# Kernel optimization log

Hardware: AMD Instinct MI355X
Metric: run time of the kernel (lower is better)

The kernel has to match this reference:

```python
import jax, jax.numpy as jnp
import numpy as np

EMBED_DIM = 1024
NUM_HEADS = 16
HEAD_DIM = EMBED_DIM // NUM_HEADS
NEG = -1000000000.0


def setup_inputs() -> dict:
    key = jax.random.key(0)
    ks = jax.random.split(key, 13)
    B, S, D = 4, 2048, EMBED_DIM
    scale = 1.0 / np.sqrt(D)
    inp = {
        "query": jax.random.normal(ks[0], (B, S, D), jnp.float32),
        "key": jax.random.normal(ks[1], (B, S, D), jnp.float32),
        "value": jax.random.normal(ks[2], (B, S, D), jnp.float32),
        "mask": jax.random.randint(ks[3], (B, 1, 1, S), 0, 2, jnp.int32),
        "Wq": jax.random.normal(ks[4], (D, D), jnp.float32) * scale,
        "bq": jnp.zeros((D,), jnp.float32),
        "Wk": jax.random.normal(ks[5], (D, D), jnp.float32) * scale,
        "bk": jnp.zeros((D,), jnp.float32),
        "Wv": jax.random.normal(ks[6], (D, D), jnp.float32) * scale,
        "bv": jnp.zeros((D,), jnp.float32),
        "Wo": jax.random.normal(ks[7], (D, D), jnp.float32) * scale,
        "bo": jnp.zeros((D,), jnp.float32),
    }
    return inp


def _split_heads(x):
    B, S, D = x.shape
    return x.reshape(B, S, NUM_HEADS, HEAD_DIM).transpose(0, 2, 1, 3)  # [B,H,S,hd]


def reference(query, key, value, mask, Wq, bq, Wk, bk, Wv, bv, Wo, bo):
    B, S, D = query.shape
    Q = _split_heads(query @ Wq + bq)
    K = _split_heads(key @ Wk + bk)
    V = _split_heads(value @ Wv + bv)
    scores = jnp.einsum("bhqd,bhkd->bhqk", Q, K) / jnp.sqrt(jnp.float32(HEAD_DIM))
    scores = jnp.where(mask == 0, jnp.float32(NEG), scores)
    attn = jax.nn.softmax(scores, axis=-1)
    out = jnp.einsum("bhqk,bhkd->bhqd", attn, V)
    out = out.transpose(0, 2, 1, 3).reshape(B, S, D)
    return out @ Wo + bo
```

## Files before the change

### kernel.cpp

```cpp
#include <hip/hip_runtime.h>


#define SEQ   2048
#define EDIM  1024
#define NHEAD 16
#define HDIM  64
#define NBAT  4
#define MTOK  8192

typedef __attribute__((ext_vector_type(8))) __bf16 bf16x8;
typedef __attribute__((ext_vector_type(4))) __bf16 bf16x4;
typedef __attribute__((ext_vector_type(4))) float f32x4;
typedef __attribute__((ext_vector_type(16))) float f32x16;
typedef __attribute__((ext_vector_type(8))) unsigned short us8;
typedef unsigned short u16;

#define SCL   0.1803368801111244f

__device__ __forceinline__ u16 bfbits(float f) {
    __bf16 h = (__bf16)f;
    return __builtin_bit_cast(u16, h);
}
__device__ __forceinline__ bf16x8 bc(us8 v) { return __builtin_bit_cast(bf16x8, v); }
__device__ __forceinline__ float exp2fast(float x) {
    float r;
    asm("v_exp_f32 %0, %1" : "=v"(r) : "v"(x));
    return r;
}
__device__ __forceinline__ void glds16(const void* g, void* l) {
    __builtin_amdgcn_global_load_lds(
        (const __attribute__((address_space(1))) unsigned int*)g,
        (__attribute__((address_space(3))) unsigned int*)l, 16, 0, 0);
}
#define VMCNT(n) asm volatile("s_waitcnt vmcnt(" #n ")" ::: "memory")

__global__ __launch_bounds__(256) void prep_kernel(const int* __restrict__ mask,
                                                   int* __restrict__ idxl,
                                                   int* __restrict__ cntp) {
    __shared__ int psum[257];
    const int b = blockIdx.x, t = threadIdx.x;
    const int* mp = mask + b * SEQ;
    int m8[8]; int s = 0;
#pragma unroll
    for (int i = 0; i < 8; ++i) { m8[i] = mp[t * 8 + i]; s += (m8[i] != 0); }
    psum[t + 1] = s;
    __syncthreads();
    if (t == 0) { psum[0] = 0; for (int i = 1; i <= 256; ++i) psum[i] += psum[i - 1]; }
    __syncthreads();
    int ex = psum[t];
#pragma unroll
    for (int i = 0; i < 8; ++i)
        if (m8[i] != 0) idxl[b * SEQ + (ex++)] = t * 8 + i;
    if (t == 0) cntp[b] = psum[256];
}

__global__ __launch_bounds__(256) void wtrans4_kernel(const float* __restrict__ W0,
                                                      const float* __restrict__ W1,
                                                      const float* __restrict__ W2,
                                                      const float* __restrict__ W3,
                                                      u16* __restrict__ WT) {
    __shared__ float tile[32][33];
    const int tx = threadIdx.x, ty = threadIdx.y;
    const int bx = blockIdx.x,  by = blockIdx.y, wz = blockIdx.z;
    const float* W = (wz == 0) ? W0 : (wz == 1) ? W1 : (wz == 2) ? W2 : W3;
    u16* O = WT + (size_t)wz * EDIM * EDIM;
#pragma unroll
    for (int i = 0; i < 4; ++i)
        tile[ty + i * 8][tx] = W[(size_t)(by * 32 + ty + i * 8) * EDIM + bx * 32 + tx];
    __syncthreads();
#pragma unroll
    for (int i = 0; i < 4; ++i) {
        int n = bx * 32 + ty + i * 8;
        int k = by * 32 + tx;
        O[(size_t)n * EDIM + k] = bfbits(tile[tx][ty + i * 8]);
    }
}

template <int MODE, bool AFP32, bool GATHER>
__global__ __launch_bounds__(256) void gemm_kernel(const void* __restrict__ Ap,
                                                   const u16* __restrict__ WT,
                                                   const float* __restrict__ bias,
                                                   void* __restrict__ outp,
                                                   const int* __restrict__ idxl,
                                                   const int* __restrict__ cntp,
                                                   const float oscale) {
    const int bm = blockIdx.x, bn = blockIdx.y;
    int cn = 0;
    if constexpr (GATHER) {
        cn = cntp[bm >> 4];
        if (((bm & 15) * 128) >= cn) return;
    }

    constexpr int ASZ = 128 * 32 * (AFP32 ? 4 : 2);
    __shared__ __align__(16) char Asraw[3][ASZ];
    __shared__ __align__(16) u16 Bs[3][128][32];

    const int tid  = threadIdx.x;
    const int lane = tid & 63, w = tid >> 6;
    const int g    = lane >> 4, l15 = lane & 15;
    const int wrow = w >> 1, wcol = w & 1;

    const char* pa[4];
    if constexpr (AFP32) {
        const float* A = (const float*)Ap;
#pragma unroll
        for (int t = 0; t < 4; ++t) {
            const int rloc = w * 32 + t * 8 + (lane >> 3);
            int arow;
            if constexpr (GATHER) {
                const int sloc = (bm & 15) * 128 + rloc;
                const int gi = (sloc < cn) ? idxl[(bm >> 4) * SEQ + sloc] : 0;
                arow = (bm >> 4) * SEQ + gi;
            } else arow = bm * 128 + rloc;
            const int scol = ((lane & 7) ^ (lane >> 3)) * 4;
            pa[t] = (const char*)(A + (size_t)arow * EDIM + scol);
        }
    } else {
        const u16* A = (const u16*)Ap;
#pragma unroll
        for (int t = 0; t < 2; ++t) {
            const int rloc = w * 32 + t * 16 + (lane >> 2);
            const int arow = bm * 128 + rloc;
            const int scol = ((lane & 3) ^ ((lane >> 3) & 3)) * 8;
            pa[t] = (const char*)(A + (size_t)arow * EDIM + scol);
        }
    }
    const char* pb[2];
#pragma unroll
    for (int t = 0; t < 2; ++t) {
        const int rloc = w * 32 + t * 16 + (lane >> 2);
        const int brow = bn * 128 + rloc;
        const int scol = ((lane & 3) ^ ((lane >> 3) & 3)) * 8;
        pb[t] = (const char*)(WT + (size_t)brow * EDIM + scol);
    }

    auto STAGE = [&](int bufn, int ko) {
        char* abase = &Asraw[bufn][0] + w * (AFP32 ? 4096 : 2048);
        if constexpr (AFP32) {
#pragma unroll
            for (int t = 0; t < 4; ++t)
                glds16(pa[t] + (size_t)ko * 4, abase + t * 1024);
        } else {
#pragma unroll
            for (int t = 0; t < 2; ++t)
                glds16(pa[t] + (size_t)ko * 2, abase + t * 1024);
        }
        char* bbase = (char*)&Bs[bufn][0][0] + w * 2048;
#pragma unroll
        for (int t = 0; t < 2; ++t)
            glds16(pb[t] + (size_t)ko * 2, bbase + t * 1024);
    };

    f32x4 acc[4][4] = {};
    constexpr int NT = EDIM / 32;

    STAGE(0, 0);
    STAGE(1, 32);
    if constexpr (AFP32) VMCNT(6); else VMCNT(4);
    __builtin_amdgcn_s_barrier();

    int bcur = 0, bn1 = 1, bn2 = 2;
#pragma unroll 1
    for (int kt = 0; kt < NT; ++kt) {
        if (kt + 2 < NT) STAGE(bn2, (kt + 2) * 32);

        bf16x8 af[4], bfr[4];
        if constexpr (AFP32) {
            const float* As = (const float*)&Asraw[bcur][0];
            const int x = l15 & 7;
#pragma unroll
            for (int i = 0; i < 4; ++i) {
                const int row = wrow * 64 + i * 16 + l15;
                f32x4 u0 = *(const f32x4*)(As + row * 32 + (((2 * g)     ^ x) * 4));
                f32x4 u1 = *(const f32x4*)(As + row * 32 + (((2 * g + 1) ^ x) * 4));
#pragma unroll
                for (int j = 0; j < 4; ++j) {
                    af[i][j]     = (__bf16)u0[j];
                    af[i][4 + j] = (__bf16)u1[j];
                }
            }
        } else {
            const u16* As = (const u16*)&Asraw[bcur][0];
            const int x = (l15 >> 1) & 3;
#pragma unroll
            for (int i = 0; i < 4; ++i) {
                const int row = wrow * 64 + i * 16 + l15;
                af[i] = bc(*(const us8*)(As + row * 32 + ((g ^ x) * 8)));
            }
        }
        {
            const int x = (l15 >> 1) & 3;
#pragma unroll
            for (int j = 0; j < 4; ++j) {
                const int row = wcol * 64 + j * 16 + l15;
                bfr[j] = bc(*(const us8*)((const u16*)&Bs[bcur][0][0] + row * 32 + ((g ^ x) * 8)));
            }
        }

#pragma unroll
        for (int i = 0; i < 4; ++i)
#pragma unroll
            for (int j = 0; j < 4; ++j)
                acc[i][j] = __builtin_amdgcn_mfma_f32_16x16x32_bf16(af[i], bfr[j], acc[i][j], 0, 0, 0);

        if (kt + 1 < NT) {
            if (kt + 2 < NT) {
                if constexpr (AFP32) VMCNT(6); else VMCNT(4);
            } else {
                VMCNT(0);
            }
            __builtin_amdgcn_s_barrier();
        }
        const int t = bcur; bcur = bn1; bn1 = bn2; bn2 = t;
    }

#pragma unroll
    for (int i = 0; i < 4; ++i) {
#pragma unroll
        for (int j = 0; j < 4; ++j) {
            const int gm0 = bm * 128 + wrow * 64 + i * 16 + g * 4;
            const int gn  = bn * 128 + wcol * 64 + j * 16 + l15;
            const float bv = bias[gn];
#pragma unroll
            for (int r = 0; r < 4; ++r) {
                float val = (acc[i][j][r] + bv) * oscale;
                const int m = gm0 + r;
                if constexpr (GATHER) {
                    if ((m & 2047) >= cn) val = 0.f;
                }
                if constexpr (MODE == 2) {
                    ((float*)outp)[(size_t)m * EDIM + gn] = val;
                } else {
                    const int b = m >> 11, s = m & 2047;
                    const int h = gn >> 6, d = gn & 63;
                    u16* O = (u16*)outp;
                    if constexpr (MODE == 0)
                        O[((size_t)(b * NHEAD + h) << 17) + s * HDIM + d] = bfbits(val);
                    else
                        O[((size_t)(b * NHEAD + h) << 17) + d * SEQ + s] = bfbits(val);
                }
            }
        }
    }
}

__global__ __launch_bounds__(256) void attn_kernel(const u16* __restrict__ Q,
                                                   const u16* __restrict__ K,
                                                   const u16* __restrict__ VT,
                                                   const int* __restrict__ cntp,
                                                   u16* __restrict__ O) {
    __shared__ u16 Klds[3][64][64];
    __shared__ u16 Vlds[3][64][64];

    const int tid = threadIdx.x, lane = tid & 63, w = tid >> 6;
    const int h = lane >> 5, l31 = lane & 31;

    const int id  = blockIdx.x;
    const int bh  = (id & 7) * 8 + ((id >> 3) >> 4);
    const int qb  = (id >> 3) & 15;
    const int b   = bh >> 4, hd_ = bh & 15;

    const u16* Qp = Q + ((size_t)bh << 17);
    const u16* Kp = K + ((size_t)bh << 17);
    const u16* Vp = VT + ((size_t)bh << 17);
    const int q0w = qb * 128 + w * 32;

    const int cn  = cntp[b];
    const int ktc = (cn + 63) >> 6;

    bf16x8 qf[4];
#pragma unroll
    for (int khd = 0; khd < 4; ++khd)
        qf[khd] = bc(*(const us8*)&Qp[(size_t)(q0w + l31) * HDIM + khd * 16 + h * 8]);

    const int b_  = l31 & 3, hp = (l31 >> 2) & 1, cc = l31 >> 3;
    const int piR = 16 * (cc & 1) + 8 * hp + 4 * (cc >> 1) + b_;
    const int swk = (piR & 3) ^ (((piR >> 3) & 3) << 1);
    const int swv = l31 & 7;

    const int lr = lane >> 3, lg = lane & 7;
    const u16* pKs[2]; const u16* pVs[2];
#pragma unroll
    for (int t = 0; t < 2; ++t) {
        const int rloc = w * 16 + t * 8 + lr;
        const int xk = (rloc & 3) ^ (((rloc >> 3) & 3) << 1);
        pKs[t] = Kp + (size_t)rloc * HDIM + ((lg ^ xk) << 3);
        const int xv = rloc & 7;
        pVs[t] = Vp + (size_t)rloc * SEQ + ((lg ^ xv) << 3);
    }

    auto STAGE = [&](int bufn, int kb) {
#pragma unroll
        for (int t = 0; t < 2; ++t) {
            glds16(pKs[t] + (size_t)kb * HDIM, &Klds[bufn][w * 16 + t * 8][0]);
            glds16(pVs[t] + kb,                &Vlds[bufn][w * 16 + t * 8][0]);
        }
    };

    f32x16 ot[2] = {};
    f32x16 ls = {};

    bf16x8 onesf;
#pragma unroll
    for (int j = 0; j < 8; ++j) onesf[j] = (__bf16)1.0f;

    STAGE(0, 0);
    if (ktc > 1) { STAGE(1, 64); VMCNT(4); } else { VMCNT(0); }
    __builtin_amdgcn_s_barrier();

    int bcur = 0, bn1 = 1, bn2 = 2;
    for (int kt = 0; kt < ktc; ++kt) {
        if (kt + 2 < ktc) STAGE(bn2, (kt + 2) * 64);

        f32x16 st[2] = {};
        __builtin_amdgcn_s_setprio(1);
#pragma unroll
        for (int kb2 = 0; kb2 < 2; ++kb2) {
            const u16* Kr = &Klds[bcur][kb2 * 32 + piR][0];
#pragma unroll
            for (int khd = 0; khd < 4; ++khd) {
                bf16x8 kf = bc(*(const us8*)&Kr[(khd * 16 + h * 8) ^ (swk << 3)]);
                st[kb2] = __builtin_amdgcn_mfma_f32_32x32x16_bf16(kf, qf[khd], st[kb2], 0, 0, 0);
            }
        }
        __builtin_amdgcn_s_setprio(0);

#pragma unroll
        for (int kb2 = 0; kb2 < 2; ++kb2)
#pragma unroll
            for (int e = 0; e < 16; ++e)
                st[kb2][e] = exp2fast(st[kb2][e]);

        if (kt == ktc - 1) {
            const int kbase = kt * 64;
#pragma unroll
            for (int kb2 = 0; kb2 < 2; ++kb2)
#pragma unroll
                for (int cp = 0; cp < 4; ++cp)
#pragma unroll
                    for (int j = 0; j < 4; ++j) {
                        const int key = kbase + kb2 * 32 + 16 * (cp & 1) + 4 * (cp >> 1) + 8 * h + j;
                        if (key >= cn) st[kb2][cp * 4 + j] = 0.f;
                    }
        }

        bf16x8 pf[4];
#pragma unroll
        for (int s = 0; s < 4; ++s) {
            const int kb2 = s >> 1, sel = (s & 1) * 4;
#pragma unroll
            for (int j = 0; j < 4; ++j) {
                pf[s][j]     = (__bf16)st[kb2][sel + j];
                pf[s][4 + j] = (__bf16)st[kb2][8 + sel + j];
            }
        }

        __builtin_amdgcn_s_setprio(1);
#pragma unroll
        for (int s = 0; s < 4; ++s)
            ls = __builtin_amdgcn_mfma_f32_32x32x16_bf16(onesf, pf[s], ls, 0, 0, 0);
#pragma unroll
        for (int dblk = 0; dblk < 2; ++dblk) {
            const u16* Vr = &Vlds[bcur][dblk * 32 + l31][0];
#pragma unroll
            for (int s = 0; s < 4; ++s) {
                bf16x8 vf = bc(*(const us8*)&Vr[(s * 16 + h * 8) ^ (swv << 3)]);
                ot[dblk] = __builtin_amdgcn_mfma_f32_32x32x16_bf16(vf, pf[s], ot[dblk], 0, 0, 0);
            }
        }
        __builtin_amdgcn_s_setprio(0);

        if (kt + 1 < ktc) {
            if (kt + 2 < ktc) { VMCNT(4); } else { VMCNT(0); }
            __builtin_amdgcn_s_barrier();
        }
        const int t = bcur; bcur = bn1; bn1 = bn2; bn2 = t;
    }

    const float inv = 1.f / ls[0];

    const size_t row = (size_t)(b * SEQ + q0w + l31) * EDIM + hd_ * HDIM;
#pragma unroll
    for (int dblk = 0; dblk < 2; ++dblk) {
#pragma unroll
        for (int cp = 0; cp < 4; ++cp) {
            bf16x4 t;
#pragma unroll
            for (int j = 0; j < 4; ++j)
                t[j] = (__bf16)(ot[dblk][cp * 4 + j] * inv);
            *(bf16x4*)&O[row + dblk * 32 + 8 * cp + 4 * h] = t;
        }
    }
}

extern "C" void kernel_launch(void* const* d_in, const int* in_sizes, int n_in,
                              void* d_out, int out_size, void* d_ws, size_t ws_size,
                              hipStream_t stream) {
    const float* query = (const float*)d_in[0];
    const float* key   = (const float*)d_in[1];
    const float* value = (const float*)d_in[2];
    const int*   mask  = (const int*)d_in[3];
    const float* Wq = (const float*)d_in[4];  const float* bq = (const float*)d_in[5];
    const float* Wk = (const float*)d_in[6];  const float* bk = (const float*)d_in[7];
    const float* Wv = (const float*)d_in[8];  const float* bv = (const float*)d_in[9];
    const float* Wo = (const float*)d_in[10]; const float* bo = (const float*)d_in[11];

    char* ws = (char*)d_ws;
    const size_t WT_BYTES  = (size_t)EDIM * EDIM * 2;
    const size_t BUF_BYTES = (size_t)MTOK * EDIM * 2;
    u16* wtq   = (u16*)(ws);
    u16* wtk   = (u16*)(ws + WT_BYTES);
    u16* wtv   = (u16*)(ws + 2 * WT_BYTES);
    u16* wto   = (u16*)(ws + 3 * WT_BYTES);
    u16* Qbuf  = (u16*)(ws + 4 * WT_BYTES);
    u16* Kbuf  = (u16*)(ws + 4 * WT_BYTES + BUF_BYTES);
    u16* VTbuf = (u16*)(ws + 4 * WT_BYTES + 2 * BUF_BYTES);
    u16* Abuf  = (u16*)(ws + 4 * WT_BYTES + 3 * BUF_BYTES);
    int* idxl  = (int*)(ws + 4 * WT_BYTES + 4 * BUF_BYTES);
    int* cntp  = (int*)(ws + 4 * WT_BYTES + 4 * BUF_BYTES + (size_t)MTOK * 4);

    prep_kernel<<<NBAT, 256, 0, stream>>>(mask, idxl, cntp);

    dim3 tgrid(32, 32, 4), tblk(32, 8);
    wtrans4_kernel<<<tgrid, tblk, 0, stream>>>(Wq, Wk, Wv, Wo, wtq);

    dim3 ggrid(MTOK / 128, EDIM / 128);
    gemm_kernel<0, true,  false><<<ggrid, 256, 0, stream>>>(query, wtq, bq, Qbuf, nullptr, nullptr, 1.0f);
    gemm_kernel<0, true,  true ><<<ggrid, 256, 0, stream>>>(key,   wtk, bk, Kbuf, idxl, cntp, SCL);
    gemm_kernel<1, true,  true ><<<ggrid, 256, 0, stream>>>(value, wtv, bv, VTbuf, idxl, cntp, 1.0f);

    attn_kernel<<<1024, 256, 0, stream>>>(Qbuf, Kbuf, VTbuf, cntp, Abuf);

    gemm_kernel<2, false, false><<<ggrid, 256, 0, stream>>>(Abuf, wto, bo, (float*)d_out, nullptr, nullptr, 1.0f);
}
```

Baseline: 198.3 us.

## Load attention K/V fragments directly from global and remap GEMM block order

The attention kernel drops its triple-buffered LDS staging of K and V tiles, along with the barriers. Each wave now loads its MFMA operand fragments straight from global memory into registers every key tile. The GEMM kernels switch to a 1D grid with a grouped block-index remap, so neighbouring blocks share A rows and weight columns in cache. The attention change removes LDS traffic and synchronisation, but it gives up cross-wave reuse and prefetch overlap and exposes global load latency in each iteration.

Result: slower. 270.1 us (+36.2%).

```diff
diff --git a/kernel.cpp b/kernel.cpp
--- a/kernel.cpp
+++ b/kernel.cpp
@@ -84,7 +84,12 @@
                                                    const int* __restrict__ idxl,
                                                    const int* __restrict__ cntp,
                                                    const float oscale) {
-    const int bm = blockIdx.x, bn = blockIdx.y;
+    const int id  = blockIdx.x;
+    const int r_  = id >> 3;
+    const int grp = r_ >> 5, bnq = (r_ >> 2) & 7, bmin = r_ & 3;
+    const int bm  = (id & 7) + 8 * (grp * 4 + bmin);
+    const int bn  = bnq;
+
     int cn = 0;
     if constexpr (GATHER) {
         cn = cntp[bm >> 4];
@@ -249,9 +254,6 @@
                                                    const u16* __restrict__ VT,
                                                    const int* __restrict__ cntp,
                                                    u16* __restrict__ O) {
-    __shared__ u16 Klds[3][64][64];
-    __shared__ u16 Vlds[3][64][64];
-
     const int tid = threadIdx.x, lane = tid & 63, w = tid >> 6;
     const int h = lane >> 5, l31 = lane & 31;
 
@@ -275,27 +277,9 @@
 
     const int b_  = l31 & 3, hp = (l31 >> 2) & 1, cc = l31 >> 3;
     const int piR = 16 * (cc & 1) + 8 * hp + 4 * (cc >> 1) + b_;
-    const int swk = (piR & 3) ^ (((piR >> 3) & 3) << 1);
-    const int swv = l31 & 7;
-
-    const int lr = lane >> 3, lg = lane & 7;
-    const u16* pKs[2]; const u16* pVs[2];
-#pragma unroll
-    for (int t = 0; t < 2; ++t) {
-        const int rloc = w * 16 + t * 8 + lr;
-        const int xk = (rloc & 3) ^ (((rloc >> 3) & 3) << 1);
-        pKs[t] = Kp + (size_t)rloc * HDIM + ((lg ^ xk) << 3);
-        const int xv = rloc & 7;
-        pVs[t] = Vp + (size_t)rloc * SEQ + ((lg ^ xv) << 3);
-    }
-
-    auto STAGE = [&](int bufn, int kb) {
-#pragma unroll
-        for (int t = 0; t < 2; ++t) {
-            glds16(pKs[t] + (size_t)kb * HDIM, &Klds[bufn][w * 16 + t * 8][0]);
-            glds16(pVs[t] + kb,                &Vlds[bufn][w * 16 + t * 8][0]);
-        }
-    };
+
+    const u16* Kl = Kp + piR * HDIM + h * 8;
+    const u16* Vl = Vp + (size_t)l31 * SEQ + h * 8;
 
     f32x16 ot[2] = {};
     f32x16 ls = {};
@@ -304,25 +288,29 @@
 #pragma unroll
     for (int j = 0; j < 8; ++j) onesf[j] = (__bf16)1.0f;
 
-    STAGE(0, 0);
-    if (ktc > 1) { STAGE(1, 64); VMCNT(4); } else { VMCNT(0); }
-    __builtin_amdgcn_s_barrier();
-
-    int bcur = 0, bn1 = 1, bn2 = 2;
     for (int kt = 0; kt < ktc; ++kt) {
-        if (kt + 2 < ktc) STAGE(bn2, (kt + 2) * 64);
+        const int kb = kt * 64;
+
+        us8 kr[2][4];
+#pragma unroll
+        for (int kb2 = 0; kb2 < 2; ++kb2)
+#pragma unroll
+            for (int khd = 0; khd < 4; ++khd)
+                kr[kb2][khd] = *(const us8*)(Kl + (size_t)(kb + kb2 * 32) * HDIM + khd * 16);
+        us8 vr[2][4];
+#pragma unroll
+        for (int dblk = 0; dblk < 2; ++dblk)
+#pragma unroll
+            for (int s = 0; s < 4; ++s)
+                vr[dblk][s] = *(const us8*)(Vl + (size_t)dblk * 32 * SEQ + kb + s * 16);
 
         f32x16 st[2] = {};
         __builtin_amdgcn_s_setprio(1);
 #pragma unroll
-        for (int kb2 = 0; kb2 < 2; ++kb2) {
-            const u16* Kr = &Klds[bcur][kb2 * 32 + piR][0];
-#pragma unroll
-            for (int khd = 0; khd < 4; ++khd) {
-                bf16x8 kf = bc(*(const us8*)&Kr[(khd * 16 + h * 8) ^ (swk << 3)]);
-                st[kb2] = __builtin_amdgcn_mfma_f32_32x32x16_bf16(kf, qf[khd], st[kb2], 0, 0, 0);
-            }
-        }
+        for (int kb2 = 0; kb2 < 2; ++kb2)
+#pragma unroll
+            for (int khd = 0; khd < 4; ++khd)
+                st[kb2] = __builtin_amdgcn_mfma_f32_32x32x16_bf16(bc(kr[kb2][khd]), qf[khd], st[kb2], 0, 0, 0);
         __builtin_amdgcn_s_setprio(0);
 
 #pragma unroll
@@ -332,14 +320,13 @@
                 st[kb2][e] = exp2fast(st[kb2][e]);
 
         if (kt == ktc - 1) {
-            const int kbase = kt * 64;
 #pragma unroll
             for (int kb2 = 0; kb2 < 2; ++kb2)
 #pragma unroll
                 for (int cp = 0; cp < 4; ++cp)
 #pragma unroll
                     for (int j = 0; j < 4; ++j) {
-                        const int key = kbase + kb2 * 32 + 16 * (cp & 1) + 4 * (cp >> 1) + 8 * h + j;
+                        const int key = kb + kb2 * 32 + 16 * (cp & 1) + 4 * (cp >> 1) + 8 * h + j;
                         if (key >= cn) st[kb2][cp * 4 + j] = 0.f;
                     }
         }
@@ -360,21 +347,11 @@
         for (int s = 0; s < 4; ++s)
             ls = __builtin_amdgcn_mfma_f32_32x32x16_bf16(onesf, pf[s], ls, 0, 0, 0);
 #pragma unroll
-        for (int dblk = 0; dblk < 2; ++dblk) {
-            const u16* Vr = &Vlds[bcur][dblk * 32 + l31][0];
-#pragma unroll
-            for (int s = 0; s < 4; ++s) {
-                bf16x8 vf = bc(*(const us8*)&Vr[(s * 16 + h * 8) ^ (swv << 3)]);
-                ot[dblk] = __builtin_amdgcn_mfma_f32_32x32x16_bf16(vf, pf[s], ot[dblk], 0, 0, 0);
-            }
-        }
+        for (int dblk = 0; dblk < 2; ++dblk)
+#pragma unroll
+            for (int s = 0; s < 4; ++s)
+                ot[dblk] = __builtin_amdgcn_mfma_f32_32x32x16_bf16(bc(vr[dblk][s]), pf[s], ot[dblk], 0, 0, 0);
         __builtin_amdgcn_s_setprio(0);
-
-        if (kt + 1 < ktc) {
-            if (kt + 2 < ktc) { VMCNT(4); } else { VMCNT(0); }
-            __builtin_amdgcn_s_barrier();
-        }
-        const int t = bcur; bcur = bn1; bn1 = bn2; bn2 = t;
     }
 
     const float inv = 1.f / ls[0];
@@ -424,12 +401,11 @@
     dim3 tgrid(32, 32, 4), tblk(32, 8);
     wtrans4_kernel<<<tgrid, tblk, 0, stream>>>(Wq, Wk, Wv, Wo, wtq);
 
-    dim3 ggrid(MTOK / 128, EDIM / 128);
-    gemm_kernel<0, true,  false><<<ggrid, 256, 0, stream>>>(query, wtq, bq, Qbuf, nullptr, nullptr, 1.0f);
-    gemm_kernel<0, true,  true ><<<ggrid, 256, 0, stream>>>(key,   wtk, bk, Kbuf, idxl, cntp, SCL);
-    gemm_kernel<1, true,  true ><<<ggrid, 256, 0, stream>>>(value, wtv, bv, VTbuf, idxl, cntp, 1.0f);
+    gemm_kernel<0, true,  false><<<512, 256, 0, stream>>>(query, wtq, bq, Qbuf, nullptr, nullptr, 1.0f);
+    gemm_kernel<0, true,  true ><<<512, 256, 0, stream>>>(key,   wtk, bk, Kbuf, idxl, cntp, SCL);
+    gemm_kernel<1, true,  true ><<<512, 256, 0, stream>>>(value, wtv, bv, VTbuf, idxl, cntp, 1.0f);
 
     attn_kernel<<<1024, 256, 0, stream>>>(Qbuf, Kbuf, VTbuf, cntp, Abuf);
 
-    gemm_kernel<2, false, false><<<ggrid, 256, 0, stream>>>(Abuf, wto, bo, (float*)d_out, nullptr, nullptr, 1.0f);
-}
+    gemm_kernel<2, false, false><<<512, 256, 0, stream>>>(Abuf, wto, bo, (float*)d_out, nullptr, nullptr, 1.0f);
+}
```
